# Optimization experiments

Measured on AMD Instinct MI355X. Metric: run time of the kernel, lower is better.

The kernel has to match this reference:

```python
import jax, jax.numpy as jnp
import numpy as np

B, T, D = 64, 512, 1024
H0, H1 = 1024, 1024

def setup_inputs() -> dict:
    key = jax.random.key(0)
    k1, k2, k3 = jax.random.split(key, 3)
    # scale weights ~ 1/sqrt(fan_in) so tanh doesn't saturate
    s0 = 1.0 / np.sqrt(H0 + D)
    s1 = 1.0 / np.sqrt(H1 + H0)
    return {
        "x": jax.random.normal(k1, (B, T, D), dtype=jnp.float32),
        "W0": jax.random.normal(k2, (H0 + D, H0), dtype=jnp.float32) * s0,
        "b0": jnp.zeros((H0,), dtype=jnp.float32),
        "W1": jax.random.normal(k3, (H1 + H0, H1), dtype=jnp.float32) * s1,
        "b1": jnp.zeros((H1,), dtype=jnp.float32),
    }

def reference(x, W0, b0, W1, b1):
    batch = x.shape[0]
    h0_init = jnp.zeros((batch, W0.shape[1]), dtype=x.dtype)
    h1_init = jnp.zeros((batch, W1.shape[1]), dtype=x.dtype)

    def step(carry, xt):
        h0, h1 = carry
        # layer 0: concat(prev hidden, input) -> dense -> tanh
        h0 = jnp.tanh(jnp.concatenate([h0, xt], axis=-1) @ W0 + b0)
        # layer 1 consumes layer 0 output
        h1 = jnp.tanh(jnp.concatenate([h1, h0], axis=-1) @ W1 + b1)
        return (h0, h1), h1

    xs = jnp.swapaxes(x, 0, 1)  # [T, B, D] time-major for scan
    (h0_f, h1_f), ys = jax.lax.scan(step, (h0_init, h1_init), xs)
    outputs = jnp.swapaxes(ys, 0, 1)  # [B, T, H1]
    final_state = jnp.concatenate([h0_f, h1_f], axis=-1)  # [B, H0+H1]
    return outputs, final_state
```

## Files before the change

### kernel.cpp

```cpp
#include <hip/hip_runtime.h>
#include <cmath>


typedef unsigned short u16;
typedef unsigned int   u32;
typedef unsigned long long u64;
typedef __bf16 bf16x8 __attribute__((ext_vector_type(8)));
typedef u16    u16x8  __attribute__((ext_vector_type(8)));
typedef u16    u16x4  __attribute__((ext_vector_type(4)));
typedef float  f32x4  __attribute__((ext_vector_type(4)));

constexpr int BB = 64;
constexpr int TT = 512;
constexpr size_t SLOT   = (size_t)64 * 1024;
constexpr size_t SLAB_B = SLOT * 2;

constexpr size_t OFF_W0T = 262144;
constexpr size_t OFF_W1T = OFF_W0T + (size_t)1024 * 2048 * 2;
constexpr size_t OFF_R   = OFF_W1T + (size_t)1024 * 2048 * 2;

constexpr int LDS_REQ = 159744;

__device__ inline u16 f2bf(float f) { return __builtin_bit_cast(u16, (__bf16)f); }
__device__ inline float bf2f(u16 v) { return (float)__builtin_bit_cast(__bf16, v); }
__device__ inline float fast_tanh(float x) {
  x = fminf(15.f, fmaxf(-15.f, x));
  float e = __expf(2.f * x);
  return (e - 1.f) * __builtin_amdgcn_rcpf(e + 1.f);
}

__global__ void zero_flags(unsigned* f) {
  int i = blockIdx.x * 256 + threadIdx.x;
  if (i < 3 * 512 * 32) f[i] = 0;
}

__global__ void transpose_w(const float* __restrict__ W0,
                            const float* __restrict__ W1,
                            u16* __restrict__ wt_base) {
  __shared__ float tile[64][65];
  int bi  = blockIdx.x;
  int mat = bi >> 9;
  int t   = bi & 511;
  int tk = t & 31, tn = t >> 5;
  const float* W = mat ? W1 : W0;
  u16* Wt = wt_base + (size_t)mat * 1024 * 2048;
  int K0 = tk * 64, N0 = tn * 64;
  int tid = threadIdx.x;
  {
    int c4 = (tid & 15) * 4;
    int r  = tid >> 4;
    for (int i = 0; i < 4; ++i) {
      int kl = r + i * 16;
      float4 v = *(const float4*)(W + (size_t)(K0 + kl) * 1024 + N0 + c4);
      tile[kl][c4 + 0] = v.x; tile[kl][c4 + 1] = v.y;
      tile[kl][c4 + 2] = v.z; tile[kl][c4 + 3] = v.w;
    }
  }
  __syncthreads();
  {
    int nl = tid >> 3;
    int kc = (tid & 7) * 8;
    for (int pass = 0; pass < 2; ++pass) {
      int n = nl + pass * 32;
      u16x8 o;
      #pragma unroll
      for (int z = 0; z < 8; ++z) o[z] = f2bf(tile[kc + z][n]);
      *(u16x8*)(Wt + (size_t)(N0 + n) * 2048 + K0 + kc) = o;
    }
  }
}

__global__ void xconv(const float* __restrict__ x, u16* __restrict__ xb) {
  int bi = blockIdx.x;
  int b = bi >> 9, t = bi & 511;
  const float* src = x + ((size_t)b * TT + t) * 1024;
  u16* dst = xb + ((size_t)t * BB + b) * 1024;
  int i = threadIdx.x * 4;
  float4 v = *(const float4*)(src + i);
  u16x4 o; o[0] = f2bf(v.x); o[1] = f2bf(v.y); o[2] = f2bf(v.z); o[3] = f2bf(v.w);
  *(u16x4*)(dst + i) = o;
}

__device__ inline void poll1(unsigned* p) {
  while (__hip_atomic_load(p, __ATOMIC_RELAXED, __HIP_MEMORY_SCOPE_SYSTEM) == 0u)
    __builtin_amdgcn_s_sleep(1);
}

template<bool COHA>
__device__ inline void load_a8(const u16* Abase, size_t aoff, bf16x8* a) {
  const u16* ap = Abase + aoff;
  #pragma unroll
  for (int ks = 0; ks < 8; ++ks) {
    if constexpr (COHA) {
      u64 lo = __hip_atomic_load((u64*)(ap + ks * 32),     __ATOMIC_RELAXED, __HIP_MEMORY_SCOPE_SYSTEM);
      u64 hi = __hip_atomic_load((u64*)(ap + ks * 32 + 4), __ATOMIC_RELAXED, __HIP_MEMORY_SCOPE_SYSTEM);
      union { u64 q2[2]; bf16x8 v; } un; un.q2[0] = lo; un.q2[1] = hi;
      a[ks] = un.v;
    } else {
      a[ks] = __builtin_bit_cast(bf16x8, *(const u16x8*)(ap + ks * 32));
    }
  }
}

__device__ inline void fma8(const bf16x8* a, const u16* bp,
                            int gbase, int n15, f32x4& acc0, f32x4& acc1) {
  #pragma unroll
  for (int ks = 0; ks < 8; ++ks) {
    int g = (gbase + 4 * ks) ^ n15;
    bf16x8 b0 = __builtin_bit_cast(bf16x8, *(const u16x8*)(bp + g * 8));
    bf16x8 b1 = __builtin_bit_cast(bf16x8, *(const u16x8*)(bp + 16 * 1024 + g * 8));
    acc0 = __builtin_amdgcn_mfma_f32_16x16x32_bf16(a[ks], b0, acc0, 0, 0, 0);
    acc1 = __builtin_amdgcn_mfma_f32_16x16x32_bf16(a[ks], b1, acc1, 0, 0, 0);
  }
}

template<bool COH>
__global__ void __launch_bounds__(1024, 1)
rnn_seq(const float* __restrict__ x, const float* __restrict__ b0v,
        const float* __restrict__ b1v, float* __restrict__ out,
        unsigned* __restrict__ flags, const u16* __restrict__ W0t,
        const u16* __restrict__ W1t, u16* __restrict__ h0r,
        u16* __restrict__ h1r, u16* __restrict__ ur,
        const u16* __restrict__ xb, int use_xb) {
  constexpr int RMASK = COH ? 15 : 511;
  constexpr int UMASK = COH ? 31 : 511;
  constexpr int RING = 16, URING = 32;
  extern __shared__ u16 lds[];
  unsigned* fl_h0 = flags;
  unsigned* fl_h1 = flags + 512 * 32;
  unsigned* fl_u  = flags + 2 * 512 * 32;

  int wg = blockIdx.x, tid = threadIdx.x;
  int grp = wg >> 5, j = wg & 31;
  int n0 = j * 32;
  int lane = tid & 63, wave = tid >> 6;
  int rb = wave & 3, ksl = wave >> 2;
  int n15 = lane & 15, q = lane >> 4;
  int r0 = rb * 16;

  u16*   wlds = lds;
  float* scr  = (float*)((char*)lds + ((grp == 1) ? 131072 : 65536));
  u16*   hch  = (u16*)((char*)scr + 24576);
  u32*   uc   = (u32*)((char*)hch + 4096);

  {
    const u16* Wt = (grp == 1) ? W1t : W0t;
    int nh = (grp == 1) ? 2 : 1;
    for (int h = 0; h < nh; ++h) {
      int kb = (grp == 1) ? h * 1024 : (grp == 2 ? 1024 : 0);
      for (int idx = tid; idx < 32 * 128; idx += 1024) {
        int n = idx >> 7, g = idx & 127;
        u16x8 v = *(const u16x8*)(Wt + (size_t)(n0 + n) * 2048 + kb + g * 8);
        *(u16x8*)(wlds + h * 32768 + n * 1024 + ((g ^ (n & 15)) * 8)) = v;
      }
    }
  }
  __syncthreads();

  const size_t aoff = (size_t)(r0 + n15) * 1024 + ksl * 256 + q * 8;
  const int gbase = 32 * ksl + q;
  const u16* bp0 = wlds + n15 * 1024;
  const u16* bp1 = wlds + 32768 + n15 * 1024;

  float bia = 0.f, bib = 0.f;
  if (grp == 1) { bia = b1v[n0 + n15]; bib = b1v[n0 + n15 + 16]; }
  if (grp == 2) { bia = b0v[n0 + n15]; bib = b0v[n0 + n15 + 16]; }

  auto scr_write = [&](const f32x4& a0, const f32x4& a1) {
    int base = ((rb * 3 + ksl - 1) * 2) * 256 + (q * 4) * 16 + n15;
    #pragma unroll
    for (int i = 0; i < 4; ++i) scr[base + i * 16] = a0[i];
    #pragma unroll
    for (int i = 0; i < 4; ++i) scr[base + 256 + i * 16] = a1[i];
  };
  auto scr_sum = [&](f32x4& a0, f32x4& a1) {
    #pragma unroll
    for (int s = 0; s < 3; ++s) {
      int base = ((rb * 3 + s) * 2) * 256 + (q * 4) * 16 + n15;
      #pragma unroll
      for (int i = 0; i < 4; ++i) a0[i] += scr[base + i * 16];
      #pragma unroll
      for (int i = 0; i < 4; ++i) a1[i] += scr[base + 256 + i * 16];
    }
  };
  const int sb  = tid >> 4;
  const int scc = (tid & 15) * 2;
  auto ring_store = [&](u16* slab) {
    u32 v = ((u32*)hch)[tid];
    __hip_atomic_store((u32*)(slab + sb * 1024 + n0 + scc), v,
                       __ATOMIC_RELAXED, __HIP_MEMORY_SCOPE_SYSTEM);
  };

  const size_t FIN = (size_t)BB * TT * 1024;

  if (grp == 0) {
    for (int t = 0; t < TT; ++t) {
      if (tid < 32)      { if (t > 0)            poll1(&fl_h0[(t - 1) * 32 + tid]); }
      else if (tid < 64) {                       poll1(&fl_u [t * 32 + (tid - 32)]); }
      else if (tid < 96) { if (COH && t >= RING) poll1(&fl_h1[(t - RING) * 32 + (tid - 64)]); }
      __syncthreads();
      bf16x8 a[8];
      if (t > 0) load_a8<COH>(h0r + (size_t)((t - 1) & RMASK) * SLOT, aoff, a);
      {
        const u16* us = ur + (size_t)(t & UMASK) * SLOT;
        const u32* up = (const u32*)(us + sb * 1024 + n0 + scc);
        u32 v = COH ? __hip_atomic_load((u32*)up, __ATOMIC_RELAXED, __HIP_MEMORY_SCOPE_SYSTEM)
                    : *up;
        uc[tid] = v;
      }
      f32x4 acc0 = {0.f, 0.f, 0.f, 0.f}, acc1 = acc0;
      if (t > 0) fma8(a, bp0, gbase, n15, acc0, acc1);
      if (ksl > 0) scr_write(acc0, acc1);
      __syncthreads();
      if (ksl == 0) {
        scr_sum(acc0, acc1);
        #pragma unroll
        for (int i = 0; i < 4; ++i) {
          int b = r0 + q * 4 + i;
          float u0 = bf2f(((u16*)uc)[b * 32 + n15]);
          float u1 = bf2f(((u16*)uc)[b * 32 + n15 + 16]);
          hch[b * 32 + n15]      = f2bf(fast_tanh(acc0[i] + u0));
          hch[b * 32 + n15 + 16] = f2bf(fast_tanh(acc1[i] + u1));
        }
      }
      __syncthreads();
      ring_store(h0r + (size_t)(t & RMASK) * SLOT);
      __syncthreads();
      if (tid == 0)
        __hip_atomic_store(&fl_h0[t * 32 + j], 1u, __ATOMIC_RELAXED, __HIP_MEMORY_SCOPE_SYSTEM);
      if (t == TT - 1) {
        u32 v = ((u32*)hch)[tid];
        float2 o; o.x = bf2f((u16)(v & 0xffff)); o.y = bf2f((u16)(v >> 16));
        *(float2*)&out[FIN + (size_t)sb * 2048 + n0 + scc] = o;
      }
    }
  } else if (grp == 1) {
    for (int t = 0; t < TT; ++t) {
      if (tid < 32 && t > 0) poll1(&fl_h1[(t - 1) * 32 + tid]);
      __syncthreads();
      f32x4 acc0 = {0.f, 0.f, 0.f, 0.f}, acc1 = acc0;
      if (t > 0) {
        bf16x8 a1[8];
        load_a8<COH>(h1r + (size_t)((t - 1) & RMASK) * SLOT, aoff, a1);
        fma8(a1, bp0, gbase, n15, acc0, acc1);
      }
      if (tid < 32) poll1(&fl_h0[t * 32 + tid]);
      __syncthreads();
      {
        bf16x8 a0[8];
        load_a8<COH>(h0r + (size_t)(t & RMASK) * SLOT, aoff, a0);
        fma8(a0, bp1, gbase, n15, acc0, acc1);
      }
      if (ksl > 0) scr_write(acc0, acc1);
      __syncthreads();
      if (ksl == 0) {
        scr_sum(acc0, acc1);
        #pragma unroll
        for (int i = 0; i < 4; ++i) {
          int b = r0 + q * 4 + i;
          hch[b * 32 + n15]      = f2bf(fast_tanh(acc0[i] + bia));
          hch[b * 32 + n15 + 16] = f2bf(fast_tanh(acc1[i] + bib));
        }
      }
      __syncthreads();
      ring_store(h1r + (size_t)(t & RMASK) * SLOT);
      __syncthreads();
      if (tid == 0)
        __hip_atomic_store(&fl_h1[t * 32 + j], 1u, __ATOMIC_RELAXED, __HIP_MEMORY_SCOPE_SYSTEM);
      {
        u32 v = ((u32*)hch)[tid];
        float2 o; o.x = bf2f((u16)(v & 0xffff)); o.y = bf2f((u16)(v >> 16));
        __builtin_nontemporal_store(o.x, &out[((size_t)sb * TT + t) * 1024 + n0 + scc]);
        __builtin_nontemporal_store(o.y, &out[((size_t)sb * TT + t) * 1024 + n0 + scc + 1]);
        if (t == TT - 1)
          *(float2*)&out[FIN + (size_t)sb * 2048 + 1024 + n0 + scc] = o;
      }
    }
  } else {
    for (int t = 0; t < TT; ++t) {
      if (COH && t >= URING) {
        if (tid < 32) poll1(&fl_h0[(t - URING) * 32 + tid]);
      }
      __syncthreads();
      f32x4 acc0 = {0.f, 0.f, 0.f, 0.f}, acc1 = acc0;
      bf16x8 a[8];
      if (use_xb) {
        load_a8<false>(xb + (size_t)t * SLOT, aoff, a);
      } else {
        const float* Ap = x + ((size_t)(r0 + n15) * TT + t) * 1024 + ksl * 256 + q * 8;
        float4 f[16];
        #pragma unroll
        for (int ks = 0; ks < 8; ++ks) {
          f[2 * ks]     = *(const float4*)(Ap + ks * 32);
          f[2 * ks + 1] = *(const float4*)(Ap + ks * 32 + 4);
        }
        #pragma unroll
        for (int ks = 0; ks < 8; ++ks) {
          bf16x8 tv;
          tv[0] = (__bf16)f[2*ks].x;   tv[1] = (__bf16)f[2*ks].y;
          tv[2] = (__bf16)f[2*ks].z;   tv[3] = (__bf16)f[2*ks].w;
          tv[4] = (__bf16)f[2*ks+1].x; tv[5] = (__bf16)f[2*ks+1].y;
          tv[6] = (__bf16)f[2*ks+1].z; tv[7] = (__bf16)f[2*ks+1].w;
          a[ks] = tv;
        }
      }
      fma8(a, bp0, gbase, n15, acc0, acc1);
      if (ksl > 0) scr_write(acc0, acc1);
      __syncthreads();
      if (ksl == 0) {
        scr_sum(acc0, acc1);
        #pragma unroll
        for (int i = 0; i < 4; ++i) {
          int b = r0 + q * 4 + i;
          hch[b * 32 + n15]      = f2bf(acc0[i] + bia);
          hch[b * 32 + n15 + 16] = f2bf(acc1[i] + bib);
        }
      }
      __syncthreads();
      ring_store(ur + (size_t)(t & UMASK) * SLOT);
      __syncthreads();
      if (tid == 0)
        __hip_atomic_store(&fl_u[t * 32 + j], 1u, __ATOMIC_RELAXED, __HIP_MEMORY_SCOPE_SYSTEM);
    }
  }
}

extern "C" void kernel_launch(void* const* d_in, const int* in_sizes, int n_in,
                              void* d_out, int out_size, void* d_ws, size_t ws_size,
                              hipStream_t stream) {
  const float* x  = (const float*)d_in[0];
  const float* W0 = (const float*)d_in[1];
  const float* b0 = (const float*)d_in[2];
  const float* W1 = (const float*)d_in[3];
  const float* b1 = (const float*)d_in[4];
  float* out = (float*)d_out;
  unsigned char* ws = (unsigned char*)d_ws;

  const size_t WS_PLAIN = OFF_R + 4ull * 512 * SLAB_B;
  bool plain = ws_size >= WS_PLAIN;
  size_t nslot  = plain ? 512 : 16;
  size_t nuslot = plain ? 512 : 32;
  size_t o_h0 = OFF_R;
  size_t o_h1 = o_h0 + nslot  * SLAB_B;
  size_t o_u  = o_h1 + nslot  * SLAB_B;
  size_t o_xb = o_u  + nuslot * SLAB_B;
  int use_xb = (plain || ws_size >= o_xb + (size_t)TT * SLAB_B) ? 1 : 0;

  unsigned* flags = (unsigned*)ws;
  const u16* W0t = (const u16*)(ws + OFF_W0T);
  const u16* W1t = (const u16*)(ws + OFF_W1T);
  u16* h0r = (u16*)(ws + o_h0);
  u16* h1r = (u16*)(ws + o_h1);
  u16* ur  = (u16*)(ws + o_u);
  u16* xb  = (u16*)(ws + o_xb);

  zero_flags<<<192, 256, 0, stream>>>(flags);
  transpose_w<<<1024, 256, 0, stream>>>(W0, W1, (u16*)(ws + OFF_W0T));
  if (use_xb) xconv<<<32768, 256, 0, stream>>>(x, xb);

  (void)hipFuncSetAttribute((const void*)rnn_seq<false>,
                            hipFuncAttributeMaxDynamicSharedMemorySize, LDS_REQ);
  (void)hipFuncSetAttribute((const void*)rnn_seq<true>,
                            hipFuncAttributeMaxDynamicSharedMemorySize, LDS_REQ);

  void* args[12];
  args[0]  = (void*)&x;    args[1]  = (void*)&b0;   args[2]  = (void*)&b1;
  args[3]  = (void*)&out;  args[4]  = (void*)&flags;
  args[5]  = (void*)&W0t;  args[6]  = (void*)&W1t;
  args[7]  = (void*)&h0r;  args[8]  = (void*)&h1r;  args[9]  = (void*)&ur;
  args[10] = (void*)&xb;   args[11] = (void*)&use_xb;
  hipLaunchCooperativeKernel(plain ? (void*)rnn_seq<false> : (void*)rnn_seq<true>,
                             dim3(96), dim3(1024), args, LDS_REQ, stream);
}
```

Baseline: 4.889 ms.

## Shorten per-step critical path: all-thread K-split reduction and merged layer-1 polls

In the layer-0 and input-projection groups, every wave now writes its partial accumulators to LDS and every thread sums its two output columns directly. This removes one barrier and the staging through an intermediate LDS buffer before the ring store. Layer 1 now waits on both the h0 and h1 flags up front and splits its waves into halves, one per input source with a wider K slice each. That replaces the sequential two-phase poll/compute with a single phase. The cost is more LDS scratch traffic, and layer 1 can no longer start the h1 half before h0 arrives.

```diff
diff --git a/kernel.cpp b/kernel.cpp
--- a/kernel.cpp
+++ b/kernel.cpp
@@ -134,14 +134,14 @@
   int grp = wg >> 5, j = wg & 31;
   int n0 = j * 32;
   int lane = tid & 63, wave = tid >> 6;
-  int rb = wave & 3, ksl = wave >> 2;
+  int rb = wave & 3;
+  int ksl = wave >> 2;
   int n15 = lane & 15, q = lane >> 4;
   int r0 = rb * 16;
 
   u16*   wlds = lds;
   float* scr  = (float*)((char*)lds + ((grp == 1) ? 131072 : 65536));
   u16*   hch  = (u16*)((char*)scr + 24576);
-  u32*   uc   = (u32*)((char*)hch + 4096);
 
   {
     const u16* Wt = (grp == 1) ? W1t : W0t;
@@ -162,12 +162,24 @@
   const u16* bp0 = wlds + n15 * 1024;
   const u16* bp1 = wlds + 32768 + n15 * 1024;
 
+  const int slice = wave >> 2;
+  const int half  = slice >> 1;
+  const int ksl2  = slice & 1;
+  const size_t aoffS = (size_t)(r0 + n15) * 1024 + ksl2 * 512 + q * 8;
+  const int gbaseS = 64 * ksl2 + q;
+  const u16* bpH = half ? bp0 : bp1;
+
+  const int sb  = tid >> 4;
+  const int scc = (tid & 15) * 2;
+  const int rbT = sb >> 4, rr = sb & 15;
+
   float bia = 0.f, bib = 0.f;
   if (grp == 1) { bia = b1v[n0 + n15]; bib = b1v[n0 + n15 + 16]; }
-  if (grp == 2) { bia = b0v[n0 + n15]; bib = b0v[n0 + n15 + 16]; }
-
-  auto scr_write = [&](const f32x4& a0, const f32x4& a1) {
-    int base = ((rb * 3 + ksl - 1) * 2) * 256 + (q * 4) * 16 + n15;
+  float2 b2x = {0.f, 0.f};
+  if (grp == 2) b2x = *(const float2*)&b0v[n0 + scc];
+
+  auto scr_write = [&](int s, const f32x4& a0, const f32x4& a1) {
+    int base = ((rb * 3 + s - 1) * 2) * 256 + (q * 4) * 16 + n15;
     #pragma unroll
     for (int i = 0; i < 4; ++i) scr[base + i * 16] = a0[i];
     #pragma unroll
@@ -183,12 +195,17 @@
       for (int i = 0; i < 4; ++i) a1[i] += scr[base + 256 + i * 16];
     }
   };
-  const int sb  = tid >> 4;
-  const int scc = (tid & 15) * 2;
-  auto ring_store = [&](u16* slab) {
-    u32 v = ((u32*)hch)[tid];
-    __hip_atomic_store((u32*)(slab + sb * 1024 + n0 + scc), v,
-                       __ATOMIC_RELAXED, __HIP_MEMORY_SCOPE_SYSTEM);
+
+  auto scr_put = [&](const f32x4& a0, const f32x4& a1) {
+    int base = rb * 2048 + ksl * 512 + (q * 4) * 16 + n15;
+    #pragma unroll
+    for (int i = 0; i < 4; ++i) scr[base + i * 16] = a0[i];
+    #pragma unroll
+    for (int i = 0; i < 4; ++i) scr[base + 256 + i * 16] = a1[i];
+  };
+  auto col_sum = [&](int c2) -> float {
+    int base = rbT * 2048 + (c2 >> 4) * 256 + rr * 16 + (c2 & 15);
+    return (scr[base] + scr[base + 512]) + (scr[base + 1024] + scr[base + 1536]);
   };
 
   const size_t FIN = (size_t)BB * TT * 1024;
@@ -201,59 +218,53 @@
       __syncthreads();
       bf16x8 a[8];
       if (t > 0) load_a8<COH>(h0r + (size_t)((t - 1) & RMASK) * SLOT, aoff, a);
+      u32 uval;
       {
-        const u16* us = ur + (size_t)(t & UMASK) * SLOT;
-        const u32* up = (const u32*)(us + sb * 1024 + n0 + scc);
-        u32 v = COH ? __hip_atomic_load((u32*)up, __ATOMIC_RELAXED, __HIP_MEMORY_SCOPE_SYSTEM)
-                    : *up;
-        uc[tid] = v;
+        const u32* up = (const u32*)(ur + (size_t)(t & UMASK) * SLOT + sb * 1024 + n0 + scc);
+        uval = COH ? __hip_atomic_load((u32*)up, __ATOMIC_RELAXED, __HIP_MEMORY_SCOPE_SYSTEM)
+                   : *up;
       }
       f32x4 acc0 = {0.f, 0.f, 0.f, 0.f}, acc1 = acc0;
       if (t > 0) fma8(a, bp0, gbase, n15, acc0, acc1);
-      if (ksl > 0) scr_write(acc0, acc1);
-      __syncthreads();
-      if (ksl == 0) {
-        scr_sum(acc0, acc1);
-        #pragma unroll
-        for (int i = 0; i < 4; ++i) {
-          int b = r0 + q * 4 + i;
-          float u0 = bf2f(((u16*)uc)[b * 32 + n15]);
-          float u1 = bf2f(((u16*)uc)[b * 32 + n15 + 16]);
-          hch[b * 32 + n15]      = f2bf(fast_tanh(acc0[i] + u0));
-          hch[b * 32 + n15 + 16] = f2bf(fast_tanh(acc1[i] + u1));
-        }
-      }
-      __syncthreads();
-      ring_store(h0r + (size_t)(t & RMASK) * SLOT);
+      scr_put(acc0, acc1);
+      __syncthreads();
+      float v0 = fast_tanh(col_sum(scc)     + bf2f((u16)(uval & 0xffffu)));
+      float v1 = fast_tanh(col_sum(scc + 1) + bf2f((u16)(uval >> 16)));
+      u32 pv = (u32)f2bf(v0) | ((u32)f2bf(v1) << 16);
+      __hip_atomic_store((u32*)(h0r + (size_t)(t & RMASK) * SLOT + sb * 1024 + n0 + scc),
+                         pv, __ATOMIC_RELAXED, __HIP_MEMORY_SCOPE_SYSTEM);
       __syncthreads();
       if (tid == 0)
         __hip_atomic_store(&fl_h0[t * 32 + j], 1u, __ATOMIC_RELAXED, __HIP_MEMORY_SCOPE_SYSTEM);
       if (t == TT - 1) {
-        u32 v = ((u32*)hch)[tid];
-        float2 o; o.x = bf2f((u16)(v & 0xffff)); o.y = bf2f((u16)(v >> 16));
+        float2 o; o.x = v0; o.y = v1;
         *(float2*)&out[FIN + (size_t)sb * 2048 + n0 + scc] = o;
       }
     }
   } else if (grp == 1) {
     for (int t = 0; t < TT; ++t) {
-      if (tid < 32 && t > 0) poll1(&fl_h1[(t - 1) * 32 + tid]);
+      if (tid < 32)      { poll1(&fl_h0[t * 32 + tid]); }
+      else if (tid < 64) { if (t > 0) poll1(&fl_h1[(t - 1) * 32 + (tid - 32)]); }
       __syncthreads();
       f32x4 acc0 = {0.f, 0.f, 0.f, 0.f}, acc1 = acc0;
-      if (t > 0) {
-        bf16x8 a1[8];
-        load_a8<COH>(h1r + (size_t)((t - 1) & RMASK) * SLOT, aoff, a1);
-        fma8(a1, bp0, gbase, n15, acc0, acc1);
-      }
-      if (tid < 32) poll1(&fl_h0[t * 32 + tid]);
-      __syncthreads();
-      {
-        bf16x8 a0[8];
-        load_a8<COH>(h0r + (size_t)(t & RMASK) * SLOT, aoff, a0);
-        fma8(a0, bp1, gbase, n15, acc0, acc1);
-      }
-      if (ksl > 0) scr_write(acc0, acc1);
-      __syncthreads();
-      if (ksl == 0) {
+      if (half == 0) {
+        bf16x8 a[16];
+        const u16* s0 = h0r + (size_t)(t & RMASK) * SLOT;
+        load_a8<COH>(s0, aoffS, a);
+        load_a8<COH>(s0, aoffS + 256, a + 8);
+        fma8(a,     bpH, gbaseS,      n15, acc0, acc1);
+        fma8(a + 8, bpH, gbaseS + 32, n15, acc0, acc1);
+      } else if (t > 0) {
+        bf16x8 a[16];
+        const u16* s1 = h1r + (size_t)((t - 1) & RMASK) * SLOT;
+        load_a8<COH>(s1, aoffS, a);
+        load_a8<COH>(s1, aoffS + 256, a + 8);
+        fma8(a,     bpH, gbaseS,      n15, acc0, acc1);
+        fma8(a + 8, bpH, gbaseS + 32, n15, acc0, acc1);
+      }
+      if (slice > 0) scr_write(slice, acc0, acc1);
+      __syncthreads();
+      if (slice == 0) {
         scr_sum(acc0, acc1);
         #pragma unroll
         for (int i = 0; i < 4; ++i) {
@@ -263,13 +274,14 @@
         }
       }
       __syncthreads();
-      ring_store(h1r + (size_t)(t & RMASK) * SLOT);
+      u32 pv = ((u32*)hch)[tid];
+      __hip_atomic_store((u32*)(h1r + (size_t)(t & RMASK) * SLOT + sb * 1024 + n0 + scc),
+                         pv, __ATOMIC_RELAXED, __HIP_MEMORY_SCOPE_SYSTEM);
       __syncthreads();
       if (tid == 0)
         __hip_atomic_store(&fl_h1[t * 32 + j], 1u, __ATOMIC_RELAXED, __HIP_MEMORY_SCOPE_SYSTEM);
       {
-        u32 v = ((u32*)hch)[tid];
-        float2 o; o.x = bf2f((u16)(v & 0xffff)); o.y = bf2f((u16)(v >> 16));
+        float2 o; o.x = bf2f((u16)(pv & 0xffffu)); o.y = bf2f((u16)(pv >> 16));
         __builtin_nontemporal_store(o.x, &out[((size_t)sb * TT + t) * 1024 + n0 + scc]);
         __builtin_nontemporal_store(o.y, &out[((size_t)sb * TT + t) * 1024 + n0 + scc + 1]);
         if (t == TT - 1)
@@ -282,7 +294,6 @@
         if (tid < 32) poll1(&fl_h0[(t - URING) * 32 + tid]);
       }
       __syncthreads();
-      f32x4 acc0 = {0.f, 0.f, 0.f, 0.f}, acc1 = acc0;
       bf16x8 a[8];
       if (use_xb) {
         load_a8<false>(xb + (size_t)t * SLOT, aoff, a);
@@ -304,20 +315,15 @@
           a[ks] = tv;
         }
       }
+      f32x4 acc0 = {0.f, 0.f, 0.f, 0.f}, acc1 = acc0;
       fma8(a, bp0, gbase, n15, acc0, acc1);
-      if (ksl > 0) scr_write(acc0, acc1);
-      __syncthreads();
-      if (ksl == 0) {
-        scr_sum(acc0, acc1);
-        #pragma unroll
-        for (int i = 0; i < 4; ++i) {
-          int b = r0 + q * 4 + i;
-          hch[b * 32 + n15]      = f2bf(acc0[i] + bia);
-          hch[b * 32 + n15 + 16] = f2bf(acc1[i] + bib);
-        }
-      }
-      __syncthreads();
-      ring_store(ur + (size_t)(t & UMASK) * SLOT);
+      scr_put(acc0, acc1);
+      __syncthreads();
+      float v0 = col_sum(scc)     + b2x.x;
+      float v1 = col_sum(scc + 1) + b2x.y;
+      u32 pv = (u32)f2bf(v0) | ((u32)f2bf(v1) << 16);
+      __hip_atomic_store((u32*)(ur + (size_t)(t & UMASK) * SLOT + sb * 1024 + n0 + scc),
+                         pv, __ATOMIC_RELAXED, __HIP_MEMORY_SCOPE_SYSTEM);
       __syncthreads();
       if (tid == 0)
         __hip_atomic_store(&fl_u[t * 32 + j], 1u, __ATOMIC_RELAXED, __HIP_MEMORY_SCOPE_SYSTEM);
```

Result: no change. 4.873 ms (-0.3%).
